# Kernel optimization log

Hardware: AMD Instinct MI355X
Metric: run time of the kernel (lower is better)

The kernel has to match this reference:

```python
import jax, jax.numpy as jnp
import numpy as np

EPS = 1e-6

def setup_inputs() -> dict:
    key = jax.random.key(0)
    k1, k2 = jax.random.split(key)
    b, seq, d = 4, 512, 64
    x = jax.random.normal(k1, (b, seq, d, d), dtype=jnp.float32)
    # diagonal decay rates in (0, 1): realistic SSM decay, positive like the clamped param
    A = jax.random.uniform(k2, (d,), dtype=jnp.float32)
    return {"x": x, "A": A}

def reference(x, A):
    b, seq, d, _ = x.shape
    log_A = jnp.log(jnp.clip(A, EPS))                      # (d,)
    # cumsum over seq of the (constant-in-time) log decay, as in the original
    cs_A = jnp.cumsum(jnp.broadcast_to(log_A, (seq, d)), axis=0)  # (seq, d)
    log_M = cs_A[:, None, :] - cs_A[None, :, :]            # (t, j, d)
    idx = jnp.arange(seq)
    mask = idx[:, None] >= idx[None, :]                    # causal: t >= j
    M = jnp.where(mask[:, :, None], jnp.exp(log_M), 0.0)   # (t, j, d)
    # A is batch-independent, so M is shared across batch (same math as the original)
    out = jnp.einsum('tjr,bjrc->btrc', M, x)               # (b, seq, d, d)
    return out
```

## Files before the change

kernel.cpp:

```cpp
#include <hip/hip_runtime.h>


#define B_    4
#define SEQ_  512
#define D_    64
#define CH_   8
#define NCH_  (SEQ_ / CH_)
#define NCQ_  (D_ / 4)
#define NTHR_ (NCH_ * NCQ_)
#define PAD_  (NCQ_ + 1)

typedef float f32x4 __attribute__((ext_vector_type(4)));

__global__ __launch_bounds__(NTHR_, 1) void ssm_scan_kernel(
    const float* __restrict__ x, const float* __restrict__ A,
    float* __restrict__ out)
{
    __shared__ float4 Epad[NCH_][PAD_];

    const int blk = blockIdx.x;
    const int bi  = blk >> 6;
    const int r   = blk & 63;
    const int tid = threadIdx.x;
    const int ch  = tid >> 4;
    const int cq  = tid & 15;

    const float a = fmaxf(A[r], 1e-6f);

    const int j0 = ch * CH_;
    const size_t base = ((size_t)(bi * SEQ_ + j0) * D_ + r) * D_ + cq * 4;
    const float4* xp = (const float4*)(x + base);
    f32x4*        op = (f32x4*)(out + base);
    const int jstride4 = (D_ * D_) / 4;

    float4 loc[CH_];
    float s0 = 0.f, s1 = 0.f, s2 = 0.f, s3 = 0.f;
    #pragma unroll
    for (int t = 0; t < CH_; ++t) {
        float4 v = xp[(size_t)t * jstride4];
        s0 = fmaf(s0, a, v.x);
        s1 = fmaf(s1, a, v.y);
        s2 = fmaf(s2, a, v.z);
        s3 = fmaf(s3, a, v.w);
        loc[t] = make_float4(s0, s1, s2, s3);
    }

    #pragma unroll
    for (int t = 0; t < CH_; ++t) {
        asm volatile("" : "+v"(loc[t].x), "+v"(loc[t].y),
                         "+v"(loc[t].z), "+v"(loc[t].w));
    }

    Epad[ch][cq] = make_float4(s0, s1, s2, s3);
    __syncthreads();

    const float a2 = a * a, a4 = a2 * a2, aL = a4 * a4;

    {
        const int w = tid >> 6;
        const int m = tid & 63;
        float4 v = Epad[m][w];
        float aw = aL;
        #pragma unroll
        for (int s = 0; s < 6; ++s) {
            const int d = 1 << s;
            float ux = __shfl_up(v.x, d, 64);
            float uy = __shfl_up(v.y, d, 64);
            float uz = __shfl_up(v.z, d, 64);
            float uw = __shfl_up(v.w, d, 64);
            if (m >= d) {
                v.x = fmaf(aw, ux, v.x);
                v.y = fmaf(aw, uy, v.y);
                v.z = fmaf(aw, uz, v.z);
                v.w = fmaf(aw, uw, v.w);
            }
            aw *= aw;
        }
        Epad[m][w] = v;
    }
    __syncthreads();

    float c0 = 0.f, c1 = 0.f, c2 = 0.f, c3 = 0.f;
    if (ch > 0) {
        float4 c4 = Epad[ch - 1][cq];
        c0 = c4.x; c1 = c4.y; c2 = c4.z; c3 = c4.w;
    }

    float p = a;
    #pragma unroll
    for (int t = 0; t < CH_; ++t) {
        float4 l = loc[t];
        f32x4 o;
        o.x = fmaf(c0, p, l.x);
        o.y = fmaf(c1, p, l.y);
        o.z = fmaf(c2, p, l.z);
        o.w = fmaf(c3, p, l.w);
        __builtin_nontemporal_store(o, &op[(size_t)t * jstride4]);
        p *= a;
    }
}

extern "C" void kernel_launch(void* const* d_in, const int* in_sizes, int n_in,
                              void* d_out, int out_size, void* d_ws, size_t ws_size,
                              hipStream_t stream) {
    const float* x   = (const float*)d_in[0];
    const float* A   = (const float*)d_in[1];
    float*       out = (float*)d_out;

    dim3 grid(B_ * D_);
    dim3 block(NTHR_);
    hipLaunchKernelGGL(ssm_scan_kernel, grid, block, 0, stream, x, A, out);
}
```

Baseline: 83.22 us.

## Split sequence across blocks with decoupled lookback via workspace flags

Replaces the per-(batch, row) block, which scanned the whole 512-step sequence, with a grid of 256 blocks over (batch, 32-step sequence tile, column quarter). Each block scans four 8-step sub-chunks in shared memory, publishes its tile aggregate to a workspace buffer with a release flag, then spins on its predecessors' flags and folds their aggregates in with powers of a. The goal is to spread a contiguous sequence segment across more CUs with coalesced access, at the cost of an extra memset launch, global-memory aggregate traffic and a spin-wait that assumes all blocks are co-resident. A fallback kernel is kept for the case where no workspace is available.

After: 177.4 us. +113.2%, slower.

```diff
diff --git a/kernel.cpp b/kernel.cpp
--- a/kernel.cpp
+++ b/kernel.cpp
@@ -4,98 +4,194 @@
 #define B_    4
 #define SEQ_  512
 #define D_    64
+#define PQ_   1024
+#define NM_   16
+#define CT_   32
+#define NQ_   4
+#define QS_   256
+#define NSUB_ 4
 #define CH_   8
-#define NCH_  (SEQ_ / CH_)
-#define NCQ_  (D_ / 4)
-#define NTHR_ (NCH_ * NCQ_)
-#define PAD_  (NCQ_ + 1)
+#define NTHR_ 1024
+#define GRID_ (B_ * NM_ * NQ_)
+#define NFLAGS_ (B_ * NQ_ * NM_)
 
 typedef float f32x4 __attribute__((ext_vector_type(4)));
 
-__global__ __launch_bounds__(NTHR_, 1) void ssm_scan_kernel(
+__global__ __launch_bounds__(NTHR_, 1) void ssm_dlb2(
     const float* __restrict__ x, const float* __restrict__ A,
-    float* __restrict__ out)
+    float* __restrict__ out, float* __restrict__ E,
+    int* __restrict__ flags)
 {
-    __shared__ float4 Epad[NCH_][PAD_];
+    __shared__ f32x4 Esub[NSUB_][QS_];
 
     const int blk = blockIdx.x;
-    const int bi  = blk >> 6;
-    const int r   = blk & 63;
+    const int q   = blk & (NQ_ - 1);
+    const int m   = (blk >> 2) & (NM_ - 1);
+    const int b   = blk >> 6;
     const int tid = threadIdx.x;
-    const int ch  = tid >> 4;
-    const int cq  = tid & 15;
-
-    const float a = fmaxf(A[r], 1e-6f);
-
-    const int j0 = ch * CH_;
-    const size_t base = ((size_t)(bi * SEQ_ + j0) * D_ + r) * D_ + cq * 4;
-    const float4* xp = (const float4*)(x + base);
-    f32x4*        op = (f32x4*)(out + base);
-    const int jstride4 = (D_ * D_) / 4;
-
-    float4 loc[CH_];
+    const int ls  = tid & (QS_ - 1);
+    const int sub = tid >> 8;
+    const int slot = q * QS_ + ls;
+    const int r   = slot >> 4;
+
+    const float a  = fmaxf(A[r], 1e-6f);
+    const float a2 = a * a, a4 = a2 * a2, a8 = a4 * a4;
+    const float a16 = a8 * a8, a32 = a16 * a16;
+
+    const int j0 = m * CT_ + sub * CH_;
+    const f32x4* xp = (const f32x4*)x + (size_t)(b * SEQ_ + j0) * PQ_ + slot;
+    f32x4*       op = (f32x4*)out     + (size_t)(b * SEQ_ + j0) * PQ_ + slot;
+
+    f32x4 loc[CH_];
     float s0 = 0.f, s1 = 0.f, s2 = 0.f, s3 = 0.f;
     #pragma unroll
     for (int t = 0; t < CH_; ++t) {
-        float4 v = xp[(size_t)t * jstride4];
+        f32x4 v = __builtin_nontemporal_load(xp + (size_t)t * PQ_);
         s0 = fmaf(s0, a, v.x);
         s1 = fmaf(s1, a, v.y);
         s2 = fmaf(s2, a, v.z);
         s3 = fmaf(s3, a, v.w);
+        loc[t].x = s0; loc[t].y = s1; loc[t].z = s2; loc[t].w = s3;
+    }
+
+    f32x4 e_end; e_end.x = s0; e_end.y = s1; e_end.z = s2; e_end.w = s3;
+    Esub[sub][ls] = e_end;
+    __syncthreads();
+
+    float c0 = 0.f, c1 = 0.f, c2 = 0.f, c3 = 0.f;
+    #pragma unroll
+    for (int i = 0; i < NSUB_ - 1; ++i) {
+        const bool use = (i < sub);
+        f32x4 e = Esub[i][ls];
+        const float w = use ? a8 : 1.0f;
+        c0 = fmaf(c0, w, use ? e.x : 0.f);
+        c1 = fmaf(c1, w, use ? e.y : 0.f);
+        c2 = fmaf(c2, w, use ? e.z : 0.f);
+        c3 = fmaf(c3, w, use ? e.w : 0.f);
+    }
+
+    if (m < NM_ - 1 && sub == NSUB_ - 1) {
+        f32x4 g;
+        g.x = fmaf(c0, a8, s0);
+        g.y = fmaf(c1, a8, s1);
+        g.z = fmaf(c2, a8, s2);
+        g.w = fmaf(c3, a8, s3);
+        ((f32x4*)E)[(size_t)(b * NM_ + m) * PQ_ + slot] = g;
+    }
+    __syncthreads();
+    if (m < NM_ - 1 && tid == 0) {
+        __threadfence();
+        __hip_atomic_store(&flags[(b * NQ_ + q) * NM_ + m], 1,
+                           __ATOMIC_RELEASE, __HIP_MEMORY_SCOPE_AGENT);
+    }
+
+    float cb0 = 0.f, cb1 = 0.f, cb2 = 0.f, cb3 = 0.f;
+    if (m > 0) {
+        if (tid < 64) {
+            const int mp = tid;
+            if (mp < m) {
+                while (__hip_atomic_load(&flags[(b * NQ_ + q) * NM_ + mp],
+                       __ATOMIC_RELAXED, __HIP_MEMORY_SCOPE_AGENT) == 0) {
+                    __builtin_amdgcn_s_sleep(2);
+                }
+            }
+        }
+        __syncthreads();
+        __threadfence();
+
+        const f32x4* Eb = (const f32x4*)E + (size_t)(b * NM_) * PQ_ + slot;
+        #pragma unroll
+        for (int mp = 0; mp < NM_ - 1; ++mp) {
+            const bool use = (mp < m);
+            f32x4 e = Eb[(size_t)mp * PQ_];
+            const float w = use ? a32 : 1.0f;
+            cb0 = fmaf(cb0, w, use ? e.x : 0.f);
+            cb1 = fmaf(cb1, w, use ? e.y : 0.f);
+            cb2 = fmaf(cb2, w, use ? e.z : 0.f);
+            cb3 = fmaf(cb3, w, use ? e.w : 0.f);
+        }
+    }
+
+    float a8p = 1.f;
+    #pragma unroll
+    for (int i = 0; i < NSUB_ - 1; ++i) a8p = (i < sub) ? a8p * a8 : a8p;
+    c0 = fmaf(cb0, a8p, c0);
+    c1 = fmaf(cb1, a8p, c1);
+    c2 = fmaf(cb2, a8p, c2);
+    c3 = fmaf(cb3, a8p, c3);
+
+    float p = a;
+    #pragma unroll
+    for (int t = 0; t < CH_; ++t) {
+        f32x4 o;
+        o.x = fmaf(c0, p, loc[t].x);
+        o.y = fmaf(c1, p, loc[t].y);
+        o.z = fmaf(c2, p, loc[t].z);
+        o.w = fmaf(c3, p, loc[t].w);
+        __builtin_nontemporal_store(o, op + (size_t)t * PQ_);
+        p *= a;
+    }
+}
+
+#define CHF_  8
+#define NCHF_ (SEQ_ / CHF_)
+#define NCQF_ (D_ / 4)
+#define PADF_ (NCQF_ + 1)
+
+__global__ __launch_bounds__(1024, 1) void ssm_fallback(
+    const float* __restrict__ x, const float* __restrict__ A,
+    float* __restrict__ out)
+{
+    __shared__ float4 Epad[NCHF_][PADF_];
+    const int blk = blockIdx.x, bi = blk >> 6, r = blk & 63;
+    const int tid = threadIdx.x, ch = tid >> 4, cq = tid & 15;
+    const float a = fmaxf(A[r], 1e-6f);
+    const size_t base = ((size_t)(bi * SEQ_ + ch * CHF_) * D_ + r) * D_ + cq * 4;
+    const float4* xp = (const float4*)(x + base);
+    f32x4*        op = (f32x4*)(out + base);
+    const int js4 = (D_ * D_) / 4;
+    float4 loc[CHF_];
+    float s0 = 0.f, s1 = 0.f, s2 = 0.f, s3 = 0.f;
+    #pragma unroll
+    for (int t = 0; t < CHF_; ++t) {
+        float4 v = xp[(size_t)t * js4];
+        s0 = fmaf(s0, a, v.x); s1 = fmaf(s1, a, v.y);
+        s2 = fmaf(s2, a, v.z); s3 = fmaf(s3, a, v.w);
         loc[t] = make_float4(s0, s1, s2, s3);
     }
-
-    #pragma unroll
-    for (int t = 0; t < CH_; ++t) {
-        asm volatile("" : "+v"(loc[t].x), "+v"(loc[t].y),
-                         "+v"(loc[t].z), "+v"(loc[t].w));
-    }
-
     Epad[ch][cq] = make_float4(s0, s1, s2, s3);
     __syncthreads();
-
     const float a2 = a * a, a4 = a2 * a2, aL = a4 * a4;
-
     {
-        const int w = tid >> 6;
-        const int m = tid & 63;
-        float4 v = Epad[m][w];
+        const int w = tid >> 6, mm = tid & 63;
+        float4 v = Epad[mm][w];
         float aw = aL;
         #pragma unroll
         for (int s = 0; s < 6; ++s) {
             const int d = 1 << s;
-            float ux = __shfl_up(v.x, d, 64);
-            float uy = __shfl_up(v.y, d, 64);
-            float uz = __shfl_up(v.z, d, 64);
-            float uw = __shfl_up(v.w, d, 64);
-            if (m >= d) {
-                v.x = fmaf(aw, ux, v.x);
-                v.y = fmaf(aw, uy, v.y);
-                v.z = fmaf(aw, uz, v.z);
-                v.w = fmaf(aw, uw, v.w);
+            float ux = __shfl_up(v.x, d, 64), uy = __shfl_up(v.y, d, 64);
+            float uz = __shfl_up(v.z, d, 64), uw = __shfl_up(v.w, d, 64);
+            if (mm >= d) {
+                v.x = fmaf(aw, ux, v.x); v.y = fmaf(aw, uy, v.y);
+                v.z = fmaf(aw, uz, v.z); v.w = fmaf(aw, uw, v.w);
             }
             aw *= aw;
         }
-        Epad[m][w] = v;
-    }
-    __syncthreads();
-
+        Epad[mm][w] = v;
+    }
+    __syncthreads();
     float c0 = 0.f, c1 = 0.f, c2 = 0.f, c3 = 0.f;
     if (ch > 0) {
         float4 c4 = Epad[ch - 1][cq];
         c0 = c4.x; c1 = c4.y; c2 = c4.z; c3 = c4.w;
     }
-
     float p = a;
     #pragma unroll
-    for (int t = 0; t < CH_; ++t) {
-        float4 l = loc[t];
+    for (int t = 0; t < CHF_; ++t) {
         f32x4 o;
-        o.x = fmaf(c0, p, l.x);
-        o.y = fmaf(c1, p, l.y);
-        o.z = fmaf(c2, p, l.z);
-        o.w = fmaf(c3, p, l.w);
-        __builtin_nontemporal_store(o, &op[(size_t)t * jstride4]);
+        o.x = fmaf(c0, p, loc[t].x); o.y = fmaf(c1, p, loc[t].y);
+        o.z = fmaf(c2, p, loc[t].z); o.w = fmaf(c3, p, loc[t].w);
+        __builtin_nontemporal_store(o, &op[(size_t)t * js4]);
         p *= a;
     }
 }
@@ -107,7 +203,17 @@
     const float* A   = (const float*)d_in[1];
     float*       out = (float*)d_out;
 
-    dim3 grid(B_ * D_);
-    dim3 block(NTHR_);
-    hipLaunchKernelGGL(ssm_scan_kernel, grid, block, 0, stream, x, A, out);
+    const size_t eBytes = sizeof(float) * (size_t)B_ * NM_ * PQ_ * 4;
+    const size_t fBytes = sizeof(int) * (size_t)NFLAGS_;
+
+    if (d_ws != nullptr && ws_size >= eBytes + fBytes) {
+        float* E     = (float*)d_ws;
+        int*   flags = (int*)((char*)d_ws + eBytes);
+        hipMemsetAsync(flags, 0, fBytes, stream);
+        hipLaunchKernelGGL(ssm_dlb2, dim3(GRID_), dim3(NTHR_), 0, stream,
+                           x, A, out, E, flags);
+    } else {
+        hipLaunchKernelGGL(ssm_fallback, dim3(B_ * D_), dim3(NTHR_),
+                           0, stream, x, A, out);
+    }
 }
```
